# Kernel optimization log

Measured on AMD Instinct MI355X. Metric: run time of the kernel, lower is better.

Reference implementation:

```python
import jax, jax.numpy as jnp
import numpy as np

HEADS = 12
C = 384
FS = 56
WS = 7
WN = FS // WS            # windows per side = 8
NW = WN * WN             # total windows = 64
DISP = WS // 2           # cyclic shift displacement = 3
DK = (C / HEADS) ** (-0.5)


def _create_mask(ws, d, zero_dim=False, one_dim=False):
    m = np.zeros((ws * ws, ws * ws), np.float32)
    if zero_dim:
        m[-d * ws:, :-d * ws] = -np.inf
        m[:-d * ws, -d * ws:] = -np.inf
    if one_dim:
        t = np.zeros((ws, ws), np.float32)
        t[-d:, :-d] = -np.inf
        t[:-d, -d:] = -np.inf
        for i in range(0, ws * ws, ws):
            for j in range(0, ws * ws, ws):
                m[i:i + ws, j:j + ws] = t
    return m


def _window_mask():
    # per-window additive mask [NW, WS*WS, WS*WS] matching the torch slicing
    zm = _create_mask(WS, DISP, zero_dim=True)
    om = _create_mask(WS, DISP, one_dim=True)
    wm = np.zeros((NW, WS * WS, WS * WS), np.float32)
    wm[-WN:] += zm                 # last row of windows
    wm[WN - 1::WN] += om           # last column of windows
    return jnp.asarray(wm)


def _rel_indices():
    idx = np.array([[x, y] for x in range(WS) for y in range(WS)], np.int64)
    rel = idx[None, :, :] - idx[:, None, :] + WS - 1   # [WS^2, WS^2, 2]
    return rel


def _dconv(x, w):
    # depthwise 3x3, padding=1
    return jax.lax.conv_general_dilated(
        x, w, (1, 1), ((1, 1), (1, 1)),
        dimension_numbers=('NCHW', 'OIHW', 'NCHW'),
        feature_group_count=w.shape[0])


def _pconv(x, w, b):
    y = jax.lax.conv_general_dilated(
        x, w, (1, 1), 'VALID', dimension_numbers=('NCHW', 'OIHW', 'NCHW'))
    return y + b[None, :, None, None]


def _to_windows(t):
    # [B, C, H, W] -> [B, heads, NW, WS*WS, head_dim]
    B = t.shape[0]
    hd = C // HEADS
    t = t.reshape(B, HEADS, hd, WN, WS, WN, WS)
    t = t.transpose(0, 1, 3, 5, 4, 6, 2)
    return t.reshape(B, HEADS, NW, WS * WS, hd)


def _from_windows(t):
    # [B, heads, NW, WS*WS, head_dim] -> [B, C, H, W]
    B = t.shape[0]
    hd = C // HEADS
    t = t.reshape(B, HEADS, WN, WN, WS, WS, hd)
    t = t.transpose(0, 1, 6, 2, 4, 3, 5)
    return t.reshape(B, C, FS, FS)


def setup_inputs() -> dict:
    key = jax.random.key(0)
    ks = jax.random.split(key, 8)
    s = 0.05
    return {
        'x': jax.random.normal(ks[0], (16, C, FS, FS), jnp.float32),
        'qkv_dw': jax.random.normal(ks[1], (C, 1, 3, 3), jnp.float32) * s,
        'qkv_pw': jax.random.normal(ks[2], (3 * C, C, 1, 1), jnp.float32) * s,
        'qkv_pb': jax.random.normal(ks[3], (3 * C,), jnp.float32) * s,
        'out_dw': jax.random.normal(ks[4], (C, 1, 3, 3), jnp.float32) * s,
        'out_pw': jax.random.normal(ks[5], (C, C, 1, 1), jnp.float32) * s,
        'out_pb': jax.random.normal(ks[6], (C,), jnp.float32) * s,
        'pos_emb': jax.random.normal(ks[7], (2 * WS - 1, 2 * WS - 1), jnp.float32),
    }


def reference(x, qkv_dw, qkv_pw, qkv_pb, out_dw, out_pw, out_pb, pos_emb):
    rel = _rel_indices()
    wmask = _window_mask()

    x = jnp.roll(x, shift=(-DISP, -DISP), axis=(2, 3))       # cyclic shift
    x = _dconv(x, qkv_dw)
    qkv = _pconv(x, qkv_pw, qkv_pb)
    q, k, v = jnp.split(qkv, 3, axis=1)
    q, k, v = _to_windows(q), _to_windows(k), _to_windows(v)

    dots = jnp.einsum('bhwid,bhwjd->bhwij', q, k) * DK
    bias = pos_emb[rel[:, :, 0], rel[:, :, 1]]               # [WS^2, WS^2]
    dots = dots + bias[None, None, None] + wmask[None, None]

    attn = jax.nn.softmax(dots, axis=-1)
    out = jnp.einsum('bhwij,bhwjd->bhwid', attn, v)
    out = _from_windows(out)

    out = jnp.roll(out, shift=(DISP, DISP), axis=(2, 3))     # cyclic back shift
    out = _dconv(out, out_dw)
    out = _pconv(out, out_pw, out_pb)
    return out
```

## Files before the change

kernel.cpp:

```cpp
#include <hip/hip_runtime.h>
#include <hip/hip_bf16.h>
#include <cstddef>
#include <cstdint>

#define BQ    16
#define CC    384
#define C3    1152
#define HH    56
#define HWP   3136
#define NTOT  (BQ * HWP)
#define NHEAD 12
#define HD    32
#define WSZ   7
#define NWIN  64
#define WSQ   49
#define DKS   0.17677669529663687f

typedef __attribute__((ext_vector_type(8))) short bf16x8;
typedef __attribute__((ext_vector_type(4))) float f32x4;

union U128 { uint4 u; bf16x8 v; ushort us[8]; uint ui[4]; };

__device__ __forceinline__ ushort f2b(float f) {
    __hip_bfloat16 h = __float2bfloat16(f);
    return *reinterpret_cast<ushort*>(&h);
}
__device__ __forceinline__ float b2f(ushort u) {
    __hip_bfloat16 h;
    *reinterpret_cast<ushort*>(&h) = u;
    return __bfloat162float(h);
}

__global__ void cvt_bf16(const float* __restrict__ in, ushort* __restrict__ out, int n) {
    const int i = blockIdx.x * 256 + threadIdx.x;
    if (i < n) out[i] = f2b(in[i]);
}

__global__ void prep_mask(const float* __restrict__ pos, float* __restrict__ M) {
    const int idx = blockIdx.x * 256 + threadIdx.x;
    const int v = idx >> 12, rem = idx & 4095;
    const int j = rem >> 6, i = rem & 63;
    float m = -1e30f;
    if (i < WSQ && j < WSQ) {
        const int pir = i / WSZ, pic = i - pir * WSZ;
        const int pjr = j / WSZ, pjc = j - pjr * WSZ;
        const bool msk = ((v & 2) && ((pir >= 4) != (pjr >= 4))) ||
                         ((v & 1) && ((pic >= 4) != (pjc >= 4)));
        m = msk ? -1e30f : pos[(pjr - pir + 6) * 13 + (pjc - pic + 6)];
    }
    M[idx] = m;
}

template <bool BF16IN, int S>
__global__ __launch_bounds__(256) void dconv_px(const void* __restrict__ inv,
                                                const float* __restrict__ dw,
                                                ushort* __restrict__ out) {
    __shared__ ushort pl[6][32][68];
    const int band = blockIdx.x, cg = blockIdx.y, b = blockIdx.z;
    const int i0 = band * 4;
    const int t = threadIdx.x;
    const int ch = t & 31;

    float wreg[9];
    #pragma unroll
    for (int k = 0; k < 9; ++k) wreg[k] = dw[(cg * 32 + ch) * 9 + k];

    if (BF16IN) {
        const ushort* src = (const ushort*)inv;
        const int c8 = t & 3, sc = t >> 2;
        const int cc = sc < 56 ? sc : sc - 56;
        #pragma unroll
        for (int lr = 0; lr < 6; ++lr) {
            const int gi = i0 + lr - 1;
            U128 u; u.u = make_uint4(0, 0, 0, 0);
            if (gi >= 0 && gi < HH) {
                int rr = gi + S; if (rr >= HH) rr -= HH;
                u.u = *(const uint4*)&src[(size_t)(b * HWP + rr * HH + cc) * CC + cg * 32 + c8 * 8];
            }
            #pragma unroll
            for (int k2 = 0; k2 < 8; ++k2) pl[lr][c8 * 8 + k2][sc] = u.us[k2];
        }
    } else {
        const float* src = (const float*)inv;
        const int cq = t & 15, q0 = t >> 4;
        const int scb = cq < 14 ? cq * 4 : cq * 4 - 56;
        #pragma unroll
        for (int k = 0; k < 12; ++k) {
            const int pair = q0 + k * 16;
            const int lc = pair & 31, lr = pair >> 5;
            const int gi = i0 + lr - 1;
            float4 v = make_float4(0.f, 0.f, 0.f, 0.f);
            if (gi >= 0 && gi < HH) {
                int rr = gi + S; if (rr >= HH) rr -= HH;
                v = *(const float4*)&src[((size_t)(b * CC + cg * 32 + lc)) * HWP + rr * HH + scb];
            }
            ushort4 w;
            w.x = f2b(v.x); w.y = f2b(v.y); w.z = f2b(v.z); w.w = f2b(v.w);
            *(ushort4*)&pl[lr][lc][cq * 4] = w;
        }
    }
    __syncthreads();

    const int u = t >> 5;
    #pragma unroll
    for (int iter = 0; iter < 7; ++iter) {
        const int unit = iter * 8 + u;
        const int colb = unit >> 2;
        const int row  = unit & 3;
        const int c0 = colb * 4;
        int sc0 = c0 - 1 + S; if (sc0 >= HH) sc0 -= HH;
        float acc[4] = {0.f, 0.f, 0.f, 0.f};
        #pragma unroll
        for (int di = 0; di < 3; ++di) {
            const ushort* rp = &pl[row + di][ch][0];
            float v[6];
            #pragma unroll
            for (int k = 0; k < 6; ++k) v[k] = b2f(rp[sc0 + k]);
            if (colb == 0)  v[0] = 0.f;
            if (colb == 13) v[5] = 0.f;
            #pragma unroll
            for (int cc2 = 0; cc2 < 4; ++cc2) {
                acc[cc2] += wreg[di * 3 + 0] * v[cc2];
                acc[cc2] += wreg[di * 3 + 1] * v[cc2 + 1];
                acc[cc2] += wreg[di * 3 + 2] * v[cc2 + 2];
            }
        }
        const int orow = i0 + row;
        #pragma unroll
        for (int cc2 = 0; cc2 < 4; ++cc2)
            out[(size_t)(b * HWP + orow * HH + c0 + cc2) * CC + cg * 32 + ch] = f2b(acc[cc2]);
    }
}

template <int OC, bool OUT_BF16>
__global__ __launch_bounds__(256) void pconv_mfma(const ushort* __restrict__ bt,
                                                  const ushort* __restrict__ wa,
                                                  const float* __restrict__ bias,
                                                  void* __restrict__ outv) {
    __shared__ __align__(16) char smem[65536];

    const int nwg = gridDim.x;
    const int cpx = nwg >> 3;
    const int id  = blockIdx.x;
    const int wg  = (id & 7) * cpx + (id >> 3);
    const int oc0 = (wg % (OC / 128)) * 128;
    const int n0  = (wg / (OC / 128)) * 128;

    const int t   = threadIdx.x;
    const int l   = t & 63;
    const int wm  = (t >> 6) >> 1, wn = (t >> 6) & 1;
    const int i15 = l & 15, g = l >> 4;

    f32x4 acc[4][4] = {};

    const int r0 = t >> 2;
    const int kc = ((t & 3) ^ ((t >> 3) & 3)) * 8;
    const size_t gA0 = (size_t)(oc0 + r0) * CC + kc;
    const size_t gA1 = (size_t)(oc0 + r0 + 64) * CC + kc;
    const size_t gB0 = (size_t)(n0 + r0) * CC + kc;
    const size_t gB1 = (size_t)(n0 + r0 + 64) * CC + kc;
    const int ldsOff = (t & 192) * 16;

#define STAGE(buf, k0) do {                                                              \
    char* la_ = smem + (buf) * 16384 + ldsOff;                                           \
    char* lb_ = la_ + 8192;                                                              \
    __builtin_amdgcn_global_load_lds(                                                    \
        (const __attribute__((address_space(1))) void*)(wa + gA0 + (k0)),                \
        (__attribute__((address_space(3))) void*)la_, 16, 0, 0);                         \
    __builtin_amdgcn_global_load_lds(                                                    \
        (const __attribute__((address_space(1))) void*)(wa + gA1 + (k0)),                \
        (__attribute__((address_space(3))) void*)(la_ + 4096), 16, 0, 0);                \
    __builtin_amdgcn_global_load_lds(                                                    \
        (const __attribute__((address_space(1))) void*)(bt + gB0 + (k0)),                \
        (__attribute__((address_space(3))) void*)lb_, 16, 0, 0);                         \
    __builtin_amdgcn_global_load_lds(                                                    \
        (const __attribute__((address_space(1))) void*)(bt + gB1 + (k0)),                \
        (__attribute__((address_space(3))) void*)(lb_ + 4096), 16, 0, 0);                \
} while (0)

    const int colb = (g ^ ((i15 >> 1) & 3)) << 4;
    const int rbA = (wm * 64 + i15) * 64 + colb;
    const int rbB = (wn * 64 + i15) * 64 + colb;

    STAGE(0, 0);
    STAGE(1, 32);

    for (int kt = 0; kt < 12; ++kt) {
        const int kS = (kt + 2) % 12;
        STAGE((kt + 2) & 3, kS * 32);
        asm volatile("s_waitcnt vmcnt(8)" ::: "memory");
        __builtin_amdgcn_s_barrier();
        const char* bufA = smem + (kt & 3) * 16384;
        const char* bufB = bufA + 8192;
        bf16x8 a[4], bb[4];
        #pragma unroll
        for (int i = 0; i < 4; ++i) {
            a[i]  = *(const bf16x8*)(bufA + rbA + i * 1024);
            bb[i] = *(const bf16x8*)(bufB + rbB + i * 1024);
        }
        #pragma unroll
        for (int mf = 0; mf < 4; ++mf)
            #pragma unroll
            for (int nf = 0; nf < 4; ++nf)
                acc[mf][nf] = __builtin_amdgcn_mfma_f32_16x16x32_bf16(a[mf], bb[nf], acc[mf][nf], 0, 0, 0);
    }
#undef STAGE

    asm volatile("s_waitcnt vmcnt(0)" ::: "memory");
    __builtin_amdgcn_s_barrier();

    const int rl = (l >> 4) * 4;
    const int cl = l & 15;
    if (OUT_BF16) {
        ushort (* const sD)[136] = (ushort(*)[136])smem;
        #pragma unroll
        for (int mf = 0; mf < 4; ++mf) {
            const int ocl = wm * 64 + mf * 16 + rl;
            #pragma unroll
            for (int nf = 0; nf < 4; ++nf) {
                const int nl = wn * 64 + nf * 16 + cl;
                ushort4 w4;
                w4.x = f2b(acc[mf][nf][0] + bias[oc0 + ocl + 0]);
                w4.y = f2b(acc[mf][nf][1] + bias[oc0 + ocl + 1]);
                w4.z = f2b(acc[mf][nf][2] + bias[oc0 + ocl + 2]);
                w4.w = f2b(acc[mf][nf][3] + bias[oc0 + ocl + 3]);
                *(ushort4*)&sD[nl][ocl] = w4;
            }
        }
        __syncthreads();
        ushort* outp = (ushort*)outv;
        #pragma unroll
        for (int rr = 0; rr < 8; ++rr) {
            const int r = (t >> 4) + rr * 16;
            const int c8 = (t & 15) * 8;
            *(uint4*)&outp[(size_t)(n0 + r) * C3 + oc0 + c8] = *(const uint4*)&sD[r][c8];
        }
    } else {
        float* outp = (float*)outv;
        #pragma unroll
        for (int mf = 0; mf < 4; ++mf) {
            const int row = oc0 + wm * 64 + mf * 16 + rl;
            #pragma unroll
            for (int r = 0; r < 4; ++r) {
                const float bs = bias[row + r];
                #pragma unroll
                for (int nf = 0; nf < 4; ++nf) {
                    const int n = n0 + wn * 64 + nf * 16 + cl;
                    const int b = n / HWP, p = n - b * HWP;
                    outp[((size_t)b * OC + row + r) * HWP + p] = acc[mf][nf][r] + bs;
                }
            }
        }
    }
}

__global__ __launch_bounds__(256) void attn_mfma(const ushort* __restrict__ qkv,
                                                 const float* __restrict__ M,
                                                 ushort* __restrict__ out) {
    __shared__ __align__(16) ushort sV[4][64 * 40];

    const int w = blockIdx.x, hg = blockIdx.y, b = blockIdx.z;
    const int wr = w >> 3, wc = w & 7;
    const int t = threadIdx.x, ww = t >> 6, l = t & 63;
    const int h = hg * 4 + ww;
    const int i15 = l & 15, g = l >> 4;
    const int hch = h * HD;
    ushort* const sVw = sV[ww];
    const float* __restrict__ Mv = M + ((((wr == 7) ? 2 : 0) | ((wc == 7) ? 1 : 0)) << 12);

    #pragma unroll
    for (int pass = 0; pass < 4; ++pass) {
        const int e = l + pass * 64;
        const int pix = e >> 2, c8 = e & 3;
        uint4 v = make_uint4(0, 0, 0, 0);
        if (pix < WSQ) {
            const int n = b * HWP + (wr * WSZ + pix / 7) * HH + wc * WSZ + pix % 7;
            v = *(const uint4*)&qkv[(size_t)n * C3 + 2 * CC + hch + c8 * 8];
        }
        const int cst = c8 ^ ((pix >> 2) & 3);
        *(uint4*)&sVw[pix * 40 + cst * 8] = v;
    }

    bf16x8 qf[4], kf[4];
    #pragma unroll
    for (int it = 0; it < 4; ++it) {
        const int i = it * 16 + i15;
        U128 uq, uk;
        uq.u = make_uint4(0, 0, 0, 0);
        uk.u = make_uint4(0, 0, 0, 0);
        if (i < WSQ) {
            const int n = b * HWP + (wr * WSZ + i / 7) * HH + wc * WSZ + i % 7;
            uq.u = *(const uint4*)&qkv[(size_t)n * C3 + hch + g * 8];
            uk.u = *(const uint4*)&qkv[(size_t)n * C3 + CC + hch + g * 8];
        }
        qf[it] = uq.v;
        kf[it] = uk.v;
    }

    f32x4 sS[4][4] = {};
    #pragma unroll
    for (int jt = 0; jt < 4; ++jt)
        #pragma unroll
        for (int it = 0; it < 4; ++it)
            sS[jt][it] = __builtin_amdgcn_mfma_f32_16x16x32_bf16(kf[jt], qf[it], sS[jt][it], 0, 0, 0);

    #pragma unroll
    for (int jt = 0; jt < 4; ++jt) {
        #pragma unroll
        for (int r = 0; r < 4; ++r) {
            const float* mrow = Mv + (jt * 16 + 4 * g + r) * 64 + i15;
            #pragma unroll
            for (int it = 0; it < 4; ++it)
                sS[jt][it][r] = fmaf(sS[jt][it][r], DKS, mrow[it * 16]);
        }
    }

    #pragma unroll
    for (int it = 0; it < 4; ++it) {
        float m = -1e30f;
        #pragma unroll
        for (int jt = 0; jt < 4; ++jt)
            #pragma unroll
            for (int r = 0; r < 4; ++r) m = fmaxf(m, sS[jt][it][r]);
        m = fmaxf(m, __shfl_xor(m, 16));
        m = fmaxf(m, __shfl_xor(m, 32));
        float sum = 0.f;
        #pragma unroll
        for (int jt = 0; jt < 4; ++jt)
            #pragma unroll
            for (int r = 0; r < 4; ++r) {
                const float e2 = __expf(sS[jt][it][r] - m);
                sS[jt][it][r] = e2;
                sum += e2;
            }
        sum += __shfl_xor(sum, 16);
        sum += __shfl_xor(sum, 32);
        const float inv = 1.f / sum;
        #pragma unroll
        for (int jt = 0; jt < 4; ++jt)
            #pragma unroll
            for (int r = 0; r < 4; ++r) sS[jt][it][r] *= inv;
    }

    uint plo[4][4], phi[4][4];
    #pragma unroll
    for (int it = 0; it < 4; ++it)
        #pragma unroll
        for (int jt = 0; jt < 4; ++jt) {
            plo[it][jt] = (uint)f2b(sS[jt][it][0]) | ((uint)f2b(sS[jt][it][1]) << 16);
            phi[it][jt] = (uint)f2b(sS[jt][it][2]) | ((uint)f2b(sS[jt][it][3]) << 16);
        }

    const int srcLo = (2 * (g & 1)) * 16 + i15;
    const int srcHi = srcLo + 16;
    const bool oddHalf = ((g >> 1) & 1) != 0;

    f32x4 oacc[4][2] = {};
    #pragma unroll
    for (int kt = 0; kt < 2; ++kt) {
        bf16x8 bv[2];
        #pragma unroll
        for (int nt = 0; nt < 2; ++nt) {
            U128 u;
            #pragma unroll
            for (int s = 0; s < 8; ++s) {
                const int j = kt * 32 + 8 * g + s;
                const int d = nt * 16 + i15;
                const int cp = (d >> 3) ^ ((j >> 2) & 3);
                u.us[s] = sVw[j * 40 + cp * 8 + (d & 7)];
            }
            bv[nt] = u.v;
        }
        #pragma unroll
        for (int mt = 0; mt < 4; ++mt) {
            U128 pu;
            #pragma unroll
            for (int u2 = 0; u2 < 4; ++u2) {
                const int sl = (u2 >> 1) ? srcHi : srcLo;
                const uint vE = __shfl((u2 & 1) ? phi[mt][2 * kt]     : plo[mt][2 * kt],     sl, 64);
                const uint vO = __shfl((u2 & 1) ? phi[mt][2 * kt + 1] : plo[mt][2 * kt + 1], sl, 64);
                pu.ui[u2] = oddHalf ? vO : vE;
            }
            #pragma unroll
            for (int nt = 0; nt < 2; ++nt)
                oacc[mt][nt] = __builtin_amdgcn_mfma_f32_16x16x32_bf16(pu.v, bv[nt], oacc[mt][nt], 0, 0, 0);
        }
    }

    #pragma unroll
    for (int mt = 0; mt < 4; ++mt)
        #pragma unroll
        for (int nt = 0; nt < 2; ++nt)
            #pragma unroll
            for (int r = 0; r < 4; ++r) {
                const int i = mt * 16 + 4 * g + r;
                const int d = nt * 16 + i15;
                const int cp = (d >> 3) ^ ((i >> 2) & 3);
                sVw[i * 40 + cp * 8 + (d & 7)] = f2b(oacc[mt][nt][r]);
            }

    #pragma unroll
    for (int pass = 0; pass < 4; ++pass) {
        const int e = l + pass * 64;
        const int pix = e >> 2, c8 = e & 3;
        if (pix < WSQ) {
            const int n = b * HWP + (wr * WSZ + pix / 7) * HH + wc * WSZ + pix % 7;
            const int cp = c8 ^ ((pix >> 2) & 3);
            *(uint4*)&out[(size_t)n * CC + hch + c8 * 8] = *(const uint4*)&sVw[pix * 40 + cp * 8];
        }
    }
}

extern "C" void kernel_launch(void* const* d_in, const int* in_sizes, int n_in,
                              void* d_out, int out_size, void* d_ws, size_t ws_size,
                              hipStream_t stream) {
    const float* x      = (const float*)d_in[0];
    const float* qkv_dw = (const float*)d_in[1];
    const float* qkv_pw = (const float*)d_in[2];
    const float* qkv_pb = (const float*)d_in[3];
    const float* out_dw = (const float*)d_in[4];
    const float* out_pw = (const float*)d_in[5];
    const float* out_pb = (const float*)d_in[6];
    const float* pos    = (const float*)d_in[7];

    ushort* A   = (ushort*)d_ws;
    ushort* B   = A + (size_t)NTOT * CC;
    ushort* wA1 = B + (size_t)NTOT * C3;
    ushort* wA2 = wA1 + (size_t)C3 * CC;
    float*  Mw  = (float*)(wA2 + (size_t)CC * CC);

    cvt_bf16<<<(C3 * CC + 255) / 256, 256, 0, stream>>>(qkv_pw, wA1, C3 * CC);
    cvt_bf16<<<(CC * CC + 255) / 256, 256, 0, stream>>>(out_pw, wA2, CC * CC);
    prep_mask<<<64, 256, 0, stream>>>(pos, Mw);

    dconv_px<false, 3><<<dim3(14, 12, BQ), 256, 0, stream>>>(x, qkv_dw, A);
    pconv_mfma<C3, true><<<dim3((C3 / 128) * (NTOT / 128)), 256, 0, stream>>>(A, wA1, qkv_pb, B);
    attn_mfma<<<dim3(NWIN, NHEAD / 4, BQ), 256, 0, stream>>>(B, Mw, A);
    dconv_px<true, 53><<<dim3(14, 12, BQ), 256, 0, stream>>>(A, out_dw, B);
    pconv_mfma<CC, false><<<dim3((CC / 128) * (NTOT / 128)), 256, 0, stream>>>(B, wA2, out_pb, (float*)d_out);
}
```

Measured before the change: 198.0 us.

## Give each wave private LDS staging to drop block barriers in pointwise GEMM

The pointwise-conv MFMA GEMM now has each wave load its own 64-row A and B slices into a private double-buffered LDS region, instead of the whole block cooperatively filling a shared 4-deep ring. This removes the per-iteration workgroup barrier, leaving only per-wave waitcnt synchronisation. The cost is redundant global loads: the wave pairs sharing wm or wn fetch the same A or B tiles, doubling load traffic. Pipelining is also shallower, with a one-stage prefetch instead of two.

```diff
diff --git a/kernel.cpp b/kernel.cpp
--- a/kernel.cpp
+++ b/kernel.cpp
@@ -148,55 +148,48 @@
 
     const int t   = threadIdx.x;
     const int l   = t & 63;
-    const int wm  = (t >> 6) >> 1, wn = (t >> 6) & 1;
+    const int w   = t >> 6;
+    const int wm  = w >> 1, wn = w & 1;
     const int i15 = l & 15, g = l >> 4;
 
     f32x4 acc[4][4] = {};
 
-    const int r0 = t >> 2;
-    const int kc = ((t & 3) ^ ((t >> 3) & 3)) * 8;
-    const size_t gA0 = (size_t)(oc0 + r0) * CC + kc;
-    const size_t gA1 = (size_t)(oc0 + r0 + 64) * CC + kc;
-    const size_t gB0 = (size_t)(n0 + r0) * CC + kc;
-    const size_t gB1 = (size_t)(n0 + r0 + 64) * CC + kc;
-    const int ldsOff = (t & 192) * 16;
-
-#define STAGE(buf, k0) do {                                                              \
-    char* la_ = smem + (buf) * 16384 + ldsOff;                                           \
-    char* lb_ = la_ + 8192;                                                              \
-    __builtin_amdgcn_global_load_lds(                                                    \
-        (const __attribute__((address_space(1))) void*)(wa + gA0 + (k0)),                \
-        (__attribute__((address_space(3))) void*)la_, 16, 0, 0);                         \
-    __builtin_amdgcn_global_load_lds(                                                    \
-        (const __attribute__((address_space(1))) void*)(wa + gA1 + (k0)),                \
-        (__attribute__((address_space(3))) void*)(la_ + 4096), 16, 0, 0);                \
-    __builtin_amdgcn_global_load_lds(                                                    \
-        (const __attribute__((address_space(1))) void*)(bt + gB0 + (k0)),                \
-        (__attribute__((address_space(3))) void*)lb_, 16, 0, 0);                         \
-    __builtin_amdgcn_global_load_lds(                                                    \
-        (const __attribute__((address_space(1))) void*)(bt + gB1 + (k0)),                \
-        (__attribute__((address_space(3))) void*)(lb_ + 4096), 16, 0, 0);                \
+    const int kcL = ((l & 3) ^ ((l >> 3) & 3)) * 8;
+    const size_t gA = (size_t)(oc0 + wm * 64 + (l >> 2)) * CC + kcL;
+    const size_t gB = (size_t)(n0  + wn * 64 + (l >> 2)) * CC + kcL;
+    char* const wbase = smem + w * 16384;
+
+#define STAGE(slot, k0) do {                                                             \
+    char* sa_ = wbase + (slot) * 8192;                                                   \
+    _Pragma("unroll")                                                                    \
+    for (int j_ = 0; j_ < 4; ++j_) {                                                     \
+        __builtin_amdgcn_global_load_lds(                                                \
+            (const __attribute__((address_space(1))) void*)(wa + gA + (size_t)j_ * 16 * CC + (k0)), \
+            (__attribute__((address_space(3))) void*)(sa_ + j_ * 1024), 16, 0, 0);       \
+        __builtin_amdgcn_global_load_lds(                                                \
+            (const __attribute__((address_space(1))) void*)(bt + gB + (size_t)j_ * 16 * CC + (k0)), \
+            (__attribute__((address_space(3))) void*)(sa_ + 4096 + j_ * 1024), 16, 0, 0);\
+    }                                                                                    \
 } while (0)
 
-    const int colb = (g ^ ((i15 >> 1) & 3)) << 4;
-    const int rbA = (wm * 64 + i15) * 64 + colb;
-    const int rbB = (wn * 64 + i15) * 64 + colb;
+    const int fb = i15 * 64 + ((g ^ ((i15 >> 1) & 3)) << 4);
 
     STAGE(0, 0);
-    STAGE(1, 32);
-
+    #pragma unroll 2
     for (int kt = 0; kt < 12; ++kt) {
-        const int kS = (kt + 2) % 12;
-        STAGE((kt + 2) & 3, kS * 32);
-        asm volatile("s_waitcnt vmcnt(8)" ::: "memory");
-        __builtin_amdgcn_s_barrier();
-        const char* bufA = smem + (kt & 3) * 16384;
-        const char* bufB = bufA + 8192;
+        if (kt < 11) {
+            asm volatile("s_waitcnt lgkmcnt(0)" ::: "memory");
+            STAGE((kt + 1) & 1, (kt + 1) * 32);
+            asm volatile("s_waitcnt vmcnt(8)" ::: "memory");
+        } else {
+            asm volatile("s_waitcnt vmcnt(0)" ::: "memory");
+        }
+        const char* sa = wbase + (kt & 1) * 8192;
         bf16x8 a[4], bb[4];
         #pragma unroll
         for (int i = 0; i < 4; ++i) {
-            a[i]  = *(const bf16x8*)(bufA + rbA + i * 1024);
-            bb[i] = *(const bf16x8*)(bufB + rbB + i * 1024);
+            a[i]  = *(const bf16x8*)(sa + fb + i * 1024);
+            bb[i] = *(const bf16x8*)(sa + 4096 + fb + i * 1024);
         }
         #pragma unroll
         for (int mf = 0; mf < 4; ++mf)
@@ -205,13 +198,11 @@
                 acc[mf][nf] = __builtin_amdgcn_mfma_f32_16x16x32_bf16(a[mf], bb[nf], acc[mf][nf], 0, 0, 0);
     }
 #undef STAGE
-
-    asm volatile("s_waitcnt vmcnt(0)" ::: "memory");
-    __builtin_amdgcn_s_barrier();
 
     const int rl = (l >> 4) * 4;
     const int cl = l & 15;
     if (OUT_BF16) {
+        __syncthreads();
         ushort (* const sD)[136] = (ushort(*)[136])smem;
         #pragma unroll
         for (int mf = 0; mf < 4; ++mf) {
```

New measurement: 215.8 us. 9.0% more time.
